# Optimization experiments

Measured on AMD Instinct MI355X. Metric: run time of the kernel, lower is better.

The kernel has to match this reference:

```python
import jax, jax.numpy as jnp
import numpy as np

N = 50000      # nodes
E = 800000     # edges
H = 4          # heads (all layers)
D = 64         # per-head out dim (n_hidden == n_classes == 64)
IN = 256       # in_feats; also H*D so identity residual is valid
NEG_SLOPE = 0.2


def setup_inputs() -> dict:
    key = jax.random.key(0)
    ks = jax.random.split(key, 16)
    x = jax.random.normal(ks[0], (N, IN), dtype=jnp.float32)
    src = jax.random.randint(ks[1], (E,), 0, N, dtype=jnp.int32)
    dst = jax.random.randint(ks[2], (E,), 0, N, dtype=jnp.int32)
    inp = {"x": x, "src": src, "dst": dst}
    fan_ins = [IN, H * D, H * D]  # layer input widths
    for i, fin in enumerate(fan_ins):
        s = 1.0 / np.sqrt(fin)
        inp[f"W{i}"] = jax.random.normal(ks[3 + 4 * i], (fin, H * D), dtype=jnp.float32) * s
        inp[f"al{i}"] = jax.random.normal(ks[4 + 4 * i], (H, D), dtype=jnp.float32) * s
        inp[f"ar{i}"] = jax.random.normal(ks[5 + 4 * i], (H, D), dtype=jnp.float32) * s
        inp[f"b{i}"] = jnp.zeros((H * D,), dtype=jnp.float32)
    return inp


def _gat_layer(h, src, dst, W, al, ar, b, residual, activate):
    # project: [N, in] @ [in, H*D] -> [N, H, D]
    feat = (h @ W).reshape(-1, H, D)
    el = jnp.sum(feat * al, axis=-1)            # [N, H]
    er = jnp.sum(feat * ar, axis=-1)            # [N, H]
    e = jax.nn.leaky_relu(el[src] + er[dst], NEG_SLOPE)  # [E, H]
    # edge softmax per destination node (stable: subtract per-dst max)
    emax = jax.ops.segment_max(e, dst, num_segments=N)  # [N, H]
    e = jnp.exp(e - emax[dst])
    denom = jax.ops.segment_sum(e, dst, num_segments=N)  # [N, H]
    alpha = e / denom[dst]                               # [E, H]
    # message + scatter-aggregate: [E, H, D] summed into [N, H, D]
    out = jax.ops.segment_sum(alpha[:, :, None] * feat[src], dst, num_segments=N)
    if residual:
        out = out + h.reshape(-1, H, D)  # identity residual (in == H*D)
    out = out + b.reshape(1, H, D)
    if activate:
        out = jax.nn.elu(out)
    return out


def reference(x, src, dst, W0, al0, ar0, b0, W1, al1, ar1, b1, W2, al2, ar2, b2):
    h = _gat_layer(x, src, dst, W0, al0, ar0, b0, False, True).reshape(N, H * D)
    h = _gat_layer(h, src, dst, W1, al1, ar1, b1, True, True).reshape(N, H * D)
    h = _gat_layer(h, src, dst, W2, al2, ar2, b2, True, False).mean(axis=1)  # [N, D]
    return h
```

## Files before the change

kernel.cpp:

```cpp
#include <hip/hip_runtime.h>
#include <math.h>

#define N_NODES 50000
#define N_EDGES 800000
#define HD 256
#define NHEAD 4
#define DH 64
#define NPAD 50048

typedef short bf16x8 __attribute__((ext_vector_type(8)));
typedef float f32x4 __attribute__((ext_vector_type(4)));

__device__ __forceinline__ unsigned short f2bf(float f) {
    unsigned u = __float_as_uint(f);
    return (unsigned short)((u + 0x7fffu + ((u >> 16) & 1u)) >> 16);
}
__device__ __forceinline__ float bf2f(unsigned short h) {
    return __uint_as_float((unsigned)h << 16);
}
__device__ __forceinline__ int origk(int k) {
    return (k & ~63) | ((k & 3) * 16 + ((k >> 2) & 15));
}

__global__ void packw_k(const float* __restrict__ W0, const float* __restrict__ W1,
                        const float* __restrict__ W2, unsigned short* __restrict__ Wp,
                        int* __restrict__ deg) {
    int blk = blockIdx.x;
    int L = blk >> 7, t = blk & 127;
    const float* W = L == 0 ? W0 : L == 1 ? W1 : W2;
    int nt = t >> 3, kt = t & 7;
    int lane = threadIdx.x;
    for (int i = blk * 64 + lane; i < 4 * NPAD; i += 384 * 64) deg[i] = 0;
    int col = nt * 16 + (lane & 15);
    int kb = kt * 32 + (lane >> 4) * 8;
    unsigned short v[8];
#pragma unroll
    for (int j = 0; j < 8; j++) {
        int k = kb + j;
        if (L > 0) k = origk(k);
        v[j] = f2bf(W[(size_t)k * 256 + col]);
    }
    *(bf16x8*)(Wp + ((size_t)(L * 128 + t) * 64 + lane) * 8) = *(bf16x8*)v;
}

__device__ __forceinline__ void mfma_tile(const unsigned short* Asl,
                                          const unsigned short* wbase,
                                          int lane, f32x4 acc[4][4]) {
#pragma unroll
    for (int kk = 0; kk < 8; kk++) {
        bf16x8 a[4], b[4];
#pragma unroll
        for (int m = 0; m < 4; m++) {
            int r = m * 16 + (lane & 15);
            int kb = kk * 32 + (lane >> 4) * 8;
            int byt = (r * 512 + kb * 2) ^ ((r & 7) << 4);
            a[m] = *(const bf16x8*)((const char*)Asl + byt);
        }
#pragma unroll
        for (int n = 0; n < 4; n++)
            b[n] = *(const bf16x8*)(wbase + ((size_t)(n * 8 + kk) * 64 + lane) * 8);
#pragma unroll
        for (int m = 0; m < 4; m++)
#pragma unroll
            for (int n = 0; n < 4; n++)
                acc[m][n] = __builtin_amdgcn_mfma_f32_16x16x32_bf16(a[m], b[n],
                                                                    acc[m][n], 0, 0, 0);
    }
}

__device__ __forceinline__ void epilogue_tile(f32x4 acc[4][4], int bm, int wv, int lane,
                                              const float* __restrict__ al,
                                              const float* __restrict__ ar,
                                              unsigned short* __restrict__ C,
                                              unsigned short* __restrict__ el,
                                              float* __restrict__ er, int M) {
    int rr = lane >> 4, cc = lane & 15;
    float alv[4], arv[4];
#pragma unroll
    for (int n = 0; n < 4; n++) {
        alv[n] = al[wv * 64 + n * 16 + cc];
        arv[n] = ar[wv * 64 + n * 16 + cc];
    }
    float vl[16], vr[16];
#pragma unroll
    for (int m = 0; m < 4; m++)
#pragma unroll
        for (int r = 0; r < 4; r++) {
            float ep = 0.f, rp = 0.f;
#pragma unroll
            for (int n = 0; n < 4; n++) {
                ep = fmaf(acc[m][n][r], alv[n], ep);
                rp = fmaf(acc[m][n][r], arv[n], rp);
            }
            vl[m * 4 + r] = ep;
            vr[m * 4 + r] = rp;
        }
    float l8[8], r8[8];
#pragma unroll
    for (int i = 0; i < 8; i++) {
        float xs = (cc & 1) ? vl[2 * i] : vl[2 * i + 1];
        float xk = (cc & 1) ? vl[2 * i + 1] : vl[2 * i];
        l8[i] = xk + __shfl_xor(xs, 1);
        float ys = (cc & 1) ? vr[2 * i] : vr[2 * i + 1];
        float yk = (cc & 1) ? vr[2 * i + 1] : vr[2 * i];
        r8[i] = yk + __shfl_xor(ys, 1);
    }
    float l4[4], r4[4];
#pragma unroll
    for (int i = 0; i < 4; i++) {
        float xs = (cc & 2) ? l8[2 * i] : l8[2 * i + 1];
        float xk = (cc & 2) ? l8[2 * i + 1] : l8[2 * i];
        l4[i] = xk + __shfl_xor(xs, 2);
        float ys = (cc & 2) ? r8[2 * i] : r8[2 * i + 1];
        float yk = (cc & 2) ? r8[2 * i + 1] : r8[2 * i];
        r4[i] = yk + __shfl_xor(ys, 2);
    }
    float l2[2], r2[2];
#pragma unroll
    for (int i = 0; i < 2; i++) {
        float xs = (cc & 4) ? l4[2 * i] : l4[2 * i + 1];
        float xk = (cc & 4) ? l4[2 * i + 1] : l4[2 * i];
        l2[i] = xk + __shfl_xor(xs, 4);
        float ys = (cc & 4) ? r4[2 * i] : r4[2 * i + 1];
        float yk = (cc & 4) ? r4[2 * i + 1] : r4[2 * i];
        r2[i] = yk + __shfl_xor(ys, 4);
    }
    {
        float xs = (cc & 8) ? l2[0] : l2[1];
        float xk = (cc & 8) ? l2[1] : l2[0];
        float lv = xk + __shfl_xor(xs, 8);
        float ys = (cc & 8) ? r2[0] : r2[1];
        float yk = (cc & 8) ? r2[1] : r2[0];
        float rv = yk + __shfl_xor(ys, 8);
        int row_e = bm + (cc >> 2) * 16 + rr * 4 + (cc & 3);
        if (row_e < M) {
            el[(size_t)row_e * NHEAD + wv] = f2bf(lv);
            er[(size_t)row_e * NHEAD + wv] = rv;
        }
    }
#pragma unroll
    for (int m = 0; m < 4; m++) {
#pragma unroll
        for (int r = 0; r < 4; r++) {
            int row = bm + m * 16 + rr * 4 + r;
            if (row < M) {
                unsigned short p4[4] = {f2bf(acc[m][0][r]), f2bf(acc[m][1][r]),
                                        f2bf(acc[m][2][r]), f2bf(acc[m][3][r])};
                *(ushort4*)(C + (size_t)row * 256 + wv * 64 + cc * 4) = *(ushort4*)p4;
            }
        }
    }
}

__global__ __launch_bounds__(256) void gemm0_k(const float* __restrict__ A,
                                               const unsigned short* __restrict__ Wp,
                                               const float* __restrict__ al,
                                               const float* __restrict__ ar,
                                               unsigned short* __restrict__ C,
                                               unsigned short* __restrict__ el,
                                               float* __restrict__ er, int M) {
    __shared__ unsigned short Asl[64 * 256];
    int tid = threadIdx.x, wv = tid >> 6, lane = tid & 63;
    int bm = blockIdx.x * 64;
#pragma unroll
    for (int i = 0; i < 8; i++) {
        int chunk = i * 256 + tid;
        int r = chunk >> 5, kc = (chunk & 31) * 8;
        float4 f0, f1;
        if (bm + r < M) {
            const float* p = A + (size_t)(bm + r) * 256 + kc;
            f0 = *(const float4*)p;
            f1 = *(const float4*)(p + 4);
        } else {
            f0 = f1 = make_float4(0.f, 0.f, 0.f, 0.f);
        }
        unsigned short tmp[8] = {f2bf(f0.x), f2bf(f0.y), f2bf(f0.z), f2bf(f0.w),
                                 f2bf(f1.x), f2bf(f1.y), f2bf(f1.z), f2bf(f1.w)};
        int b = (r * 512 + kc * 2) ^ ((r & 7) << 4);
        *(bf16x8*)((char*)Asl + b) = *(bf16x8*)tmp;
    }
    __syncthreads();
    const unsigned short* wbase = Wp + (size_t)(wv * 4) * 8 * 64 * 8;
    f32x4 acc[4][4] = {};
    mfma_tile(Asl, wbase, lane, acc);
    epilogue_tile(acc, bm, wv, lane, al, ar, C, el, er, M);
}

__global__ __launch_bounds__(256) void gemm2_k(const unsigned short* __restrict__ A,
                                               const unsigned short* __restrict__ Wp,
                                               const float* __restrict__ al,
                                               const float* __restrict__ ar,
                                               unsigned short* __restrict__ C,
                                               unsigned short* __restrict__ el,
                                               float* __restrict__ er, int M) {
    __shared__ unsigned short Asl[2][64 * 256];
    int tid = threadIdx.x, wv = tid >> 6, lane = tid & 63;
    int bm0 = blockIdx.x * 128, bm1 = bm0 + 64;
#pragma unroll
    for (int i = 0; i < 8; i++) {
        int chunk = i * 256 + tid;
        int r = chunk >> 5;
        int c16 = (chunk & 31) ^ (r & 7);
        int grow = bm0 + r; if (grow >= M) grow = M - 1;
        __builtin_amdgcn_global_load_lds(
            (const __attribute__((address_space(1))) unsigned int*)
                (A + (size_t)grow * 256 + c16 * 8),
            (__attribute__((address_space(3))) unsigned int*)
                ((char*)Asl[0] + (size_t)chunk * 16),
            16, 0, 0);
    }
#pragma unroll
    for (int i = 0; i < 8; i++) {
        int chunk = i * 256 + tid;
        int r = chunk >> 5;
        int c16 = (chunk & 31) ^ (r & 7);
        int grow = bm1 + r; if (grow >= M) grow = M - 1;
        __builtin_amdgcn_global_load_lds(
            (const __attribute__((address_space(1))) unsigned int*)
                (A + (size_t)grow * 256 + c16 * 8),
            (__attribute__((address_space(3))) unsigned int*)
                ((char*)Asl[1] + (size_t)chunk * 16),
            16, 0, 0);
    }
    asm volatile("s_waitcnt vmcnt(8)" ::: "memory");
    __builtin_amdgcn_sched_barrier(0);
    __builtin_amdgcn_s_barrier();
    const unsigned short* wbase = Wp + (size_t)(wv * 4) * 8 * 64 * 8;
    f32x4 acc[4][4] = {};
    mfma_tile(Asl[0], wbase, lane, acc);
    asm volatile("s_waitcnt vmcnt(0)" ::: "memory");
    __builtin_amdgcn_sched_barrier(0);
    __builtin_amdgcn_s_barrier();
    epilogue_tile(acc, bm0, wv, lane, al, ar, C, el, er, M);
    f32x4 acc2[4][4] = {};
    mfma_tile(Asl[1], wbase, lane, acc2);
    epilogue_tile(acc2, bm1, wv, lane, al, ar, C, el, er, M);
}

__global__ void hist_k(const int* __restrict__ dst, int* __restrict__ deg) {
    int t = blockIdx.x * 256 + threadIdx.x;
    int e = t * 2;
    int* mydeg = deg + (size_t)(threadIdx.x & 3) * NPAD;
    if (e + 1 < N_EDGES) {
        int2 d2 = *(const int2*)(dst + e);
        atomicAdd(&mydeg[d2.x], 1);
        atomicAdd(&mydeg[d2.y], 1);
    } else if (e < N_EDGES) {
        atomicAdd(&mydeg[dst[e]], 1);
    }
}

__global__ __launch_bounds__(1024) void scan1_k(const int* __restrict__ deg,
                                                int* __restrict__ rowptr,
                                                int* __restrict__ bsum) {
    __shared__ int wsum[16];
    int tid = threadIdx.x, lane = tid & 63, wv = tid >> 6;
    int i = blockIdx.x * 1024 + tid;
    int v = 0;
    if (i < N_NODES)
        v = deg[i] + deg[i + NPAD] + deg[i + 2 * NPAD] + deg[i + 3 * NPAD];
    int sc = v;
#pragma unroll
    for (int o = 1; o < 64; o <<= 1) {
        int t = __shfl_up(sc, o);
        if (lane >= o) sc += t;
    }
    if (lane == 63) wsum[wv] = sc;
    __syncthreads();
    if (wv == 0 && lane < 16) {
        int ws = wsum[lane];
#pragma unroll
        for (int o = 1; o < 16; o <<= 1) {
            int t = __shfl_up(ws, o);
            if (lane >= o) ws += t;
        }
        wsum[lane] = ws;
    }
    __syncthreads();
    int incl = sc + (wv > 0 ? wsum[wv - 1] : 0);
    if (i < N_NODES) rowptr[i + 1] = incl;
    if (tid == 1023) bsum[blockIdx.x] = incl;
}

__global__ __launch_bounds__(1024) void scan3_k(int* __restrict__ rowptr,
                                                const int* __restrict__ bsum,
                                                int* __restrict__ cursor, int nb) {
    __shared__ int boff_s;
    int tid = threadIdx.x;
    if (tid < 64) {
        int v = (tid < nb) ? bsum[tid] : 0;
        int sc = v;
#pragma unroll
        for (int o = 1; o < 64; o <<= 1) {
            int t = __shfl_up(sc, o);
            if ((tid & 63) >= o) sc += t;
        }
        if (tid == (int)blockIdx.x) boff_s = sc - v;
    }
    __syncthreads();
    int off = boff_s;
    int i = blockIdx.x * 1024 + tid;
    if (blockIdx.x == 0 && tid == 0) { rowptr[0] = 0; cursor[0] = 0; }
    if (i < N_NODES) {
        int v = rowptr[i + 1] + off;
        rowptr[i + 1] = v;
        if (i + 1 < N_NODES) cursor[i + 1] = v;
    }
}

__global__ void scatter_k(const int* __restrict__ src, const int* __restrict__ dst,
                          int* __restrict__ cursor, int* __restrict__ csr_src) {
    int e = (blockIdx.x * 256 + threadIdx.x) * 2;
    if (e + 1 < N_EDGES) {
        int2 s2 = *(const int2*)(src + e);
        int2 d2 = *(const int2*)(dst + e);
        csr_src[atomicAdd(&cursor[d2.x], 1)] = s2.x;
        csr_src[atomicAdd(&cursor[d2.y], 1)] = s2.y;
    } else if (e < N_EDGES) {
        csr_src[atomicAdd(&cursor[dst[e]], 1)] = src[e];
    }
}

template <int MODE>
__global__ __launch_bounds__(256) void agg_k(const int* __restrict__ rowptr,
                                             const int* __restrict__ csr_src,
                                             const unsigned short* __restrict__ el,
                                             const float* __restrict__ er,
                                             const unsigned short* __restrict__ feat,
                                             const unsigned short* __restrict__ resid,
                                             const float* __restrict__ bias,
                                             float* __restrict__ out,
                                             unsigned short* __restrict__ hb) {
    __shared__ int   ws_s[4][64];
    __shared__ float ws_w[4][4][68];
    int wv = threadIdx.x >> 6, lane = threadIdx.x & 63;
    int node = blockIdx.x * 4 + wv;
    if (node >= N_NODES) return;
    int beg = rowptr[node], end = rowptr[node + 1];
    float4 er4 = *(const float4*)(er + (size_t)node * 4);
    float4 acc0 = make_float4(0.f, 0.f, 0.f, 0.f);
    float4 acc1 = make_float4(0.f, 0.f, 0.f, 0.f);
    float4 den = make_float4(0.f, 0.f, 0.f, 0.f);
    int h = lane >> 4;
    int l8 = lane * 8;
    const char* fb = (const char*)feat;
    for (int base = beg; base < end; base += 64) {
        int j = base + lane;
        int soff = 0;
        float4 w = make_float4(0.f, 0.f, 0.f, 0.f);
        if (j < end) {
            int s = csr_src[j];
            soff = s << 9;
            ushort4 l4u = *(const ushort4*)(el + (size_t)s * 4);
            float vx = bf2f(l4u.x) + er4.x; vx = vx > 0.f ? vx : 0.2f * vx;
            float vy = bf2f(l4u.y) + er4.y; vy = vy > 0.f ? vy : 0.2f * vy;
            float vz = bf2f(l4u.z) + er4.z; vz = vz > 0.f ? vz : 0.2f * vz;
            float vw = bf2f(l4u.w) + er4.w; vw = vw > 0.f ? vw : 0.2f * vw;
            w.x = expf(vx); w.y = expf(vy); w.z = expf(vz); w.w = expf(vw);
            den.x += w.x; den.y += w.y; den.z += w.z; den.w += w.w;
        }
        ws_s[wv][lane] = soff;
        ws_w[wv][0][lane] = w.x;
        ws_w[wv][1][lane] = w.y;
        ws_w[wv][2][lane] = w.z;
        ws_w[wv][3][lane] = w.w;
        __builtin_amdgcn_wave_barrier();
        int cnt = end - base; if (cnt > 64) cnt = 64;
        int cnt4 = (cnt + 3) & ~3;
        for (int k = 0; k < cnt4; k += 4) {
            int4   so = *(const int4*)&ws_s[wv][k];
            float4 w4 = *(const float4*)&ws_w[wv][h][k];
            ushort4 u0 = *(const ushort4*)(fb + (so.x + l8));
            ushort4 u1 = *(const ushort4*)(fb + (so.y + l8));
            ushort4 u2 = *(const ushort4*)(fb + (so.z + l8));
            ushort4 u3 = *(const ushort4*)(fb + (so.w + l8));
            acc0.x = fmaf(w4.x, bf2f(u0.x), acc0.x);
            acc0.y = fmaf(w4.x, bf2f(u0.y), acc0.y);
            acc0.z = fmaf(w4.x, bf2f(u0.z), acc0.z);
            acc0.w = fmaf(w4.x, bf2f(u0.w), acc0.w);
            acc1.x = fmaf(w4.y, bf2f(u1.x), acc1.x);
            acc1.y = fmaf(w4.y, bf2f(u1.y), acc1.y);
            acc1.z = fmaf(w4.y, bf2f(u1.z), acc1.z);
            acc1.w = fmaf(w4.y, bf2f(u1.w), acc1.w);
            acc0.x = fmaf(w4.z, bf2f(u2.x), acc0.x);
            acc0.y = fmaf(w4.z, bf2f(u2.y), acc0.y);
            acc0.z = fmaf(w4.z, bf2f(u2.z), acc0.z);
            acc0.w = fmaf(w4.z, bf2f(u2.w), acc0.w);
            acc1.x = fmaf(w4.w, bf2f(u3.x), acc1.x);
            acc1.y = fmaf(w4.w, bf2f(u3.y), acc1.y);
            acc1.z = fmaf(w4.w, bf2f(u3.z), acc1.z);
            acc1.w = fmaf(w4.w, bf2f(u3.w), acc1.w);
        }
        __builtin_amdgcn_wave_barrier();
    }
    float4 acc;
    acc.x = acc0.x + acc1.x; acc.y = acc0.y + acc1.y;
    acc.z = acc0.z + acc1.z; acc.w = acc0.w + acc1.w;
#pragma unroll
    for (int o = 1; o < 64; o <<= 1) {
        den.x += __shfl_xor(den.x, o);
        den.y += __shfl_xor(den.y, o);
        den.z += __shfl_xor(den.z, o);
        den.w += __shfl_xor(den.w, o);
    }
    float den_me = h == 0 ? den.x : h == 1 ? den.y : h == 2 ? den.z : den.w;
    float r = den_me > 0.f ? 1.f / den_me : 0.f;
    int cc = lane & 15;
    float4 b4;
    b4.x = bias[h * 64 + 0 * 16 + cc];
    b4.y = bias[h * 64 + 1 * 16 + cc];
    b4.z = bias[h * 64 + 2 * 16 + cc];
    b4.w = bias[h * 64 + 3 * 16 + cc];
    float4 o4;
    o4.x = acc.x * r + b4.x;
    o4.y = acc.y * r + b4.y;
    o4.z = acc.z * r + b4.z;
    o4.w = acc.w * r + b4.w;
    if (MODE >= 1) {
        ushort4 r4 = *(const ushort4*)(resid + (size_t)node * HD + lane * 4);
        o4.x += bf2f(r4.x); o4.y += bf2f(r4.y);
        o4.z += bf2f(r4.z); o4.w += bf2f(r4.w);
    }
    if (MODE <= 1) {
        o4.x = o4.x > 0.f ? o4.x : expm1f(o4.x);
        o4.y = o4.y > 0.f ? o4.y : expm1f(o4.y);
        o4.z = o4.z > 0.f ? o4.z : expm1f(o4.z);
        o4.w = o4.w > 0.f ? o4.w : expm1f(o4.w);
        ushort4 hv;
        hv.x = f2bf(o4.x); hv.y = f2bf(o4.y); hv.z = f2bf(o4.z); hv.w = f2bf(o4.w);
        *(ushort4*)(hb + (size_t)node * HD + lane * 4) = hv;
    } else {
        o4.x += __shfl_xor(o4.x, 16); o4.x += __shfl_xor(o4.x, 32);
        o4.y += __shfl_xor(o4.y, 16); o4.y += __shfl_xor(o4.y, 32);
        o4.z += __shfl_xor(o4.z, 16); o4.z += __shfl_xor(o4.z, 32);
        o4.w += __shfl_xor(o4.w, 16); o4.w += __shfl_xor(o4.w, 32);
        if (lane < 16) {
            float* po = out + (size_t)node * DH;
            po[0 * 16 + lane] = o4.x * 0.25f;
            po[1 * 16 + lane] = o4.y * 0.25f;
            po[2 * 16 + lane] = o4.z * 0.25f;
            po[3 * 16 + lane] = o4.w * 0.25f;
        }
    }
}

extern "C" void kernel_launch(void* const* d_in, const int* in_sizes, int n_in,
                              void* d_out, int out_size, void* d_ws, size_t ws_size,
                              hipStream_t stream) {
    const float* x   = (const float*)d_in[0];
    const int*   src = (const int*)d_in[1];
    const int*   dst = (const int*)d_in[2];
    const float* W[3]  = {(const float*)d_in[3], (const float*)d_in[7],  (const float*)d_in[11]};
    const float* al[3] = {(const float*)d_in[4], (const float*)d_in[8],  (const float*)d_in[12]};
    const float* ar[3] = {(const float*)d_in[5], (const float*)d_in[9],  (const float*)d_in[13]};
    const float* bb[3] = {(const float*)d_in[6], (const float*)d_in[10], (const float*)d_in[14]};

    size_t big = (size_t)N_NODES * HD;
    unsigned short* featb = (unsigned short*)d_ws;
    unsigned short* hb1 = featb + big;
    unsigned short* hb2 = hb1 + big;
    unsigned short* el = hb2 + big;
    float* er = (float*)(el + (size_t)NPAD * NHEAD);
    int* deg     = (int*)(er + (size_t)NPAD * NHEAD);
    int* rowptr  = deg + 4 * NPAD;
    int* cursor  = rowptr + NPAD;
    int* csr_src = cursor + NPAD;
    int* bsum    = csr_src + N_EDGES;
    unsigned short* Wp = (unsigned short*)(bsum + 64);

    const int NB = (N_NODES + 1023) / 1024;

    packw_k<<<384, 64, 0, stream>>>(W[0], W[1], W[2], Wp, deg);
    hist_k<<<(N_EDGES / 2 + 255) / 256, 256, 0, stream>>>(dst, deg);
    scan1_k<<<NB, 1024, 0, stream>>>(deg, rowptr, bsum);
    scan3_k<<<NB, 1024, 0, stream>>>(rowptr, bsum, cursor, NB);
    scatter_k<<<(N_EDGES / 2 + 255) / 256, 256, 0, stream>>>(src, dst, cursor, csr_src);

    int g0grid = (N_NODES + 63) / 64;
    int g2grid = (N_NODES + 127) / 128;
    int agrid = (N_NODES + 3) / 4;

    gemm0_k<<<g0grid, 256, 0, stream>>>(x, Wp, al[0], ar[0], featb, el, er, N_NODES);
    agg_k<0><<<agrid, 256, 0, stream>>>(rowptr, csr_src, el, er, featb,
                                        nullptr, bb[0], nullptr, hb1);
    gemm2_k<<<g2grid, 256, 0, stream>>>(hb1, Wp + (size_t)1 * 128 * 64 * 8,
                                        al[1], ar[1], featb, el, er, N_NODES);
    agg_k<1><<<agrid, 256, 0, stream>>>(rowptr, csr_src, el, er, featb,
                                        hb1, bb[1], nullptr, hb2);
    gemm2_k<<<g2grid, 256, 0, stream>>>(hb2, Wp + (size_t)2 * 128 * 64 * 8,
                                        al[2], ar[2], featb, el, er, N_NODES);
    agg_k<2><<<agrid, 256, 0, stream>>>(rowptr, csr_src, el, er, featb,
                                        hb2, bb[2], (float*)d_out, nullptr);
}
```

Before: 327.1 us.

## Fuse weight packing with histogram and layer-0 GEMM with scan phase

Merges the weight-pack and degree-histogram kernels into one launch with block-range dispatch, and merges the layer-0 GEMM with the first scan pass. The deg zeroing moves to a memset, and the scan is now 1024 elements per 256-thread block, four per thread. The goal is fewer kernel launches and letting independent preprocessing work overlap on the GPU. The cost is a heterogeneous kernel whose shared-memory and register footprint is set by the GEMM branch, which may limit occupancy for the scan blocks.

```diff
diff --git a/kernel.cpp b/kernel.cpp
--- a/kernel.cpp
+++ b/kernel.cpp
@@ -8,6 +8,11 @@
 #define DH 64
 #define NPAD 50048
 
+#define GEMM_BLKS 782
+#define PACK_BLKS 96
+#define HIST_BLKS 1563
+#define NB 49
+
 typedef short bf16x8 __attribute__((ext_vector_type(8)));
 typedef float f32x4 __attribute__((ext_vector_type(4)));
 
@@ -20,27 +25,6 @@
 }
 __device__ __forceinline__ int origk(int k) {
     return (k & ~63) | ((k & 3) * 16 + ((k >> 2) & 15));
-}
-
-__global__ void packw_k(const float* __restrict__ W0, const float* __restrict__ W1,
-                        const float* __restrict__ W2, unsigned short* __restrict__ Wp,
-                        int* __restrict__ deg) {
-    int blk = blockIdx.x;
-    int L = blk >> 7, t = blk & 127;
-    const float* W = L == 0 ? W0 : L == 1 ? W1 : W2;
-    int nt = t >> 3, kt = t & 7;
-    int lane = threadIdx.x;
-    for (int i = blk * 64 + lane; i < 4 * NPAD; i += 384 * 64) deg[i] = 0;
-    int col = nt * 16 + (lane & 15);
-    int kb = kt * 32 + (lane >> 4) * 8;
-    unsigned short v[8];
-#pragma unroll
-    for (int j = 0; j < 8; j++) {
-        int k = kb + j;
-        if (L > 0) k = origk(k);
-        v[j] = f2bf(W[(size_t)k * 256 + col]);
-    }
-    *(bf16x8*)(Wp + ((size_t)(L * 128 + t) * 64 + lane) * 8) = *(bf16x8*)v;
 }
 
 __device__ __forceinline__ void mfma_tile(const unsigned short* Asl,
@@ -152,38 +136,151 @@
     }
 }
 
-__global__ __launch_bounds__(256) void gemm0_k(const float* __restrict__ A,
-                                               const unsigned short* __restrict__ Wp,
-                                               const float* __restrict__ al,
-                                               const float* __restrict__ ar,
-                                               unsigned short* __restrict__ C,
-                                               unsigned short* __restrict__ el,
-                                               float* __restrict__ er, int M) {
+__global__ __launch_bounds__(256) void fused_ph_k(const float* __restrict__ W0,
+                                                  const float* __restrict__ W1,
+                                                  const float* __restrict__ W2,
+                                                  unsigned short* __restrict__ Wp,
+                                                  const int* __restrict__ dst,
+                                                  int* __restrict__ deg) {
+    int blk = blockIdx.x, tid = threadIdx.x, wv = tid >> 6, lane = tid & 63;
+    if (blk < PACK_BLKS) {
+        int tile = blk * 4 + wv;
+        int L = tile >> 7, t = tile & 127;
+        const float* W = L == 0 ? W0 : L == 1 ? W1 : W2;
+        int nt = t >> 3, kt = t & 7;
+        int col = nt * 16 + (lane & 15);
+        int kb = kt * 32 + (lane >> 4) * 8;
+        unsigned short v[8];
+#pragma unroll
+        for (int j = 0; j < 8; j++) {
+            int k = kb + j;
+            if (L > 0) k = origk(k);
+            v[j] = f2bf(W[(size_t)k * 256 + col]);
+        }
+        *(bf16x8*)(Wp + ((size_t)(L * 128 + t) * 64 + lane) * 8) = *(bf16x8*)v;
+    } else {
+        int t = (blk - PACK_BLKS) * 256 + tid;
+        int e = t * 2;
+        int* mydeg = deg + (size_t)(tid & 3) * NPAD;
+        if (e + 1 < N_EDGES) {
+            int2 d2 = *(const int2*)(dst + e);
+            atomicAdd(&mydeg[d2.x], 1);
+            atomicAdd(&mydeg[d2.y], 1);
+        } else if (e < N_EDGES) {
+            atomicAdd(&mydeg[dst[e]], 1);
+        }
+    }
+}
+
+__global__ __launch_bounds__(256) void fused_gs_k(const float* __restrict__ A,
+                                                  const unsigned short* __restrict__ Wp,
+                                                  const float* __restrict__ al,
+                                                  const float* __restrict__ ar,
+                                                  unsigned short* __restrict__ C,
+                                                  unsigned short* __restrict__ el,
+                                                  float* __restrict__ er,
+                                                  const int* __restrict__ deg,
+                                                  int* __restrict__ rowptr,
+                                                  int* __restrict__ bsum, int M) {
     __shared__ unsigned short Asl[64 * 256];
-    int tid = threadIdx.x, wv = tid >> 6, lane = tid & 63;
-    int bm = blockIdx.x * 64;
-#pragma unroll
-    for (int i = 0; i < 8; i++) {
-        int chunk = i * 256 + tid;
-        int r = chunk >> 5, kc = (chunk & 31) * 8;
-        float4 f0, f1;
-        if (bm + r < M) {
-            const float* p = A + (size_t)(bm + r) * 256 + kc;
-            f0 = *(const float4*)p;
-            f1 = *(const float4*)(p + 4);
-        } else {
-            f0 = f1 = make_float4(0.f, 0.f, 0.f, 0.f);
-        }
-        unsigned short tmp[8] = {f2bf(f0.x), f2bf(f0.y), f2bf(f0.z), f2bf(f0.w),
-                                 f2bf(f1.x), f2bf(f1.y), f2bf(f1.z), f2bf(f1.w)};
-        int b = (r * 512 + kc * 2) ^ ((r & 7) << 4);
-        *(bf16x8*)((char*)Asl + b) = *(bf16x8*)tmp;
+    __shared__ int wsum2[4];
+    int blk = blockIdx.x, tid = threadIdx.x, wv = tid >> 6, lane = tid & 63;
+    if (blk < GEMM_BLKS) {
+        int bm = blk * 64;
+#pragma unroll
+        for (int i = 0; i < 8; i++) {
+            int chunk = i * 256 + tid;
+            int r = chunk >> 5, kc = (chunk & 31) * 8;
+            float4 f0, f1;
+            if (bm + r < M) {
+                const float* p = A + (size_t)(bm + r) * 256 + kc;
+                f0 = *(const float4*)p;
+                f1 = *(const float4*)(p + 4);
+            } else {
+                f0 = f1 = make_float4(0.f, 0.f, 0.f, 0.f);
+            }
+            unsigned short tmp[8] = {f2bf(f0.x), f2bf(f0.y), f2bf(f0.z), f2bf(f0.w),
+                                     f2bf(f1.x), f2bf(f1.y), f2bf(f1.z), f2bf(f1.w)};
+            int b = (r * 512 + kc * 2) ^ ((r & 7) << 4);
+            *(bf16x8*)((char*)Asl + b) = *(bf16x8*)tmp;
+        }
+        __syncthreads();
+        const unsigned short* wbase = Wp + (size_t)(wv * 4) * 8 * 64 * 8;
+        f32x4 acc[4][4] = {};
+        mfma_tile(Asl, wbase, lane, acc);
+        epilogue_tile(acc, bm, wv, lane, al, ar, C, el, er, M);
+    } else {
+        int sblk = blk - GEMM_BLKS;
+        int i0 = sblk * 1024 + tid * 4;
+        int v[4], p[4];
+#pragma unroll
+        for (int j = 0; j < 4; j++) {
+            int i = i0 + j;
+            v[j] = (i < N_NODES)
+                       ? deg[i] + deg[i + NPAD] + deg[i + 2 * NPAD] + deg[i + 3 * NPAD]
+                       : 0;
+        }
+        p[0] = v[0]; p[1] = p[0] + v[1]; p[2] = p[1] + v[2]; p[3] = p[2] + v[3];
+        int tot = p[3];
+        int sc = tot;
+#pragma unroll
+        for (int o = 1; o < 64; o <<= 1) {
+            int t = __shfl_up(sc, o);
+            if (lane >= o) sc += t;
+        }
+        if (lane == 63) wsum2[wv] = sc;
+        __syncthreads();
+        int woff = 0;
+#pragma unroll
+        for (int w = 0; w < 4; w++)
+            if (w < wv) woff += wsum2[w];
+        int excl = woff + sc - tot;
+#pragma unroll
+        for (int j = 0; j < 4; j++) {
+            int i = i0 + j;
+            if (i < N_NODES) rowptr[i + 1] = excl + p[j];
+        }
+        if (tid == 255) bsum[sblk] = excl + p[3];
+    }
+}
+
+__global__ __launch_bounds__(1024) void scan3_k(int* __restrict__ rowptr,
+                                                const int* __restrict__ bsum,
+                                                int* __restrict__ cursor, int nb) {
+    __shared__ int boff_s;
+    int tid = threadIdx.x;
+    if (tid < 64) {
+        int v = (tid < nb) ? bsum[tid] : 0;
+        int sc = v;
+#pragma unroll
+        for (int o = 1; o < 64; o <<= 1) {
+            int t = __shfl_up(sc, o);
+            if ((tid & 63) >= o) sc += t;
+        }
+        if (tid == (int)blockIdx.x) boff_s = sc - v;
     }
     __syncthreads();
-    const unsigned short* wbase = Wp + (size_t)(wv * 4) * 8 * 64 * 8;
-    f32x4 acc[4][4] = {};
-    mfma_tile(Asl, wbase, lane, acc);
-    epilogue_tile(acc, bm, wv, lane, al, ar, C, el, er, M);
+    int off = boff_s;
+    int i = blockIdx.x * 1024 + tid;
+    if (blockIdx.x == 0 && tid == 0) { rowptr[0] = 0; cursor[0] = 0; }
+    if (i < N_NODES) {
+        int v = rowptr[i + 1] + off;
+        rowptr[i + 1] = v;
+        if (i + 1 < N_NODES) cursor[i + 1] = v;
+    }
+}
+
+__global__ void scatter_k(const int* __restrict__ src, const int* __restrict__ dst,
+                          int* __restrict__ cursor, int* __restrict__ csr_src) {
+    int e = (blockIdx.x * 256 + threadIdx.x) * 2;
+    if (e + 1 < N_EDGES) {
+        int2 s2 = *(const int2*)(src + e);
+        int2 d2 = *(const int2*)(dst + e);
+        csr_src[atomicAdd(&cursor[d2.x], 1)] = s2.x;
+        csr_src[atomicAdd(&cursor[d2.y], 1)] = s2.y;
+    } else if (e < N_EDGES) {
+        csr_src[atomicAdd(&cursor[dst[e]], 1)] = src[e];
+    }
 }
 
 __global__ __launch_bounds__(256) void gemm2_k(const unsigned short* __restrict__ A,
@@ -235,90 +332,6 @@
     f32x4 acc2[4][4] = {};
     mfma_tile(Asl[1], wbase, lane, acc2);
     epilogue_tile(acc2, bm1, wv, lane, al, ar, C, el, er, M);
-}
-
-__global__ void hist_k(const int* __restrict__ dst, int* __restrict__ deg) {
-    int t = blockIdx.x * 256 + threadIdx.x;
-    int e = t * 2;
-    int* mydeg = deg + (size_t)(threadIdx.x & 3) * NPAD;
-    if (e + 1 < N_EDGES) {
-        int2 d2 = *(const int2*)(dst + e);
-        atomicAdd(&mydeg[d2.x], 1);
-        atomicAdd(&mydeg[d2.y], 1);
-    } else if (e < N_EDGES) {
-        atomicAdd(&mydeg[dst[e]], 1);
-    }
-}
-
-__global__ __launch_bounds__(1024) void scan1_k(const int* __restrict__ deg,
-                                                int* __restrict__ rowptr,
-                                                int* __restrict__ bsum) {
-    __shared__ int wsum[16];
-    int tid = threadIdx.x, lane = tid & 63, wv = tid >> 6;
-    int i = blockIdx.x * 1024 + tid;
-    int v = 0;
-    if (i < N_NODES)
-        v = deg[i] + deg[i + NPAD] + deg[i + 2 * NPAD] + deg[i + 3 * NPAD];
-    int sc = v;
-#pragma unroll
-    for (int o = 1; o < 64; o <<= 1) {
-        int t = __shfl_up(sc, o);
-        if (lane >= o) sc += t;
-    }
-    if (lane == 63) wsum[wv] = sc;
-    __syncthreads();
-    if (wv == 0 && lane < 16) {
-        int ws = wsum[lane];
-#pragma unroll
-        for (int o = 1; o < 16; o <<= 1) {
-            int t = __shfl_up(ws, o);
-            if (lane >= o) ws += t;
-        }
-        wsum[lane] = ws;
-    }
-    __syncthreads();
-    int incl = sc + (wv > 0 ? wsum[wv - 1] : 0);
-    if (i < N_NODES) rowptr[i + 1] = incl;
-    if (tid == 1023) bsum[blockIdx.x] = incl;
-}
-
-__global__ __launch_bounds__(1024) void scan3_k(int* __restrict__ rowptr,
-                                                const int* __restrict__ bsum,
-                                                int* __restrict__ cursor, int nb) {
-    __shared__ int boff_s;
-    int tid = threadIdx.x;
-    if (tid < 64) {
-        int v = (tid < nb) ? bsum[tid] : 0;
-        int sc = v;
-#pragma unroll
-        for (int o = 1; o < 64; o <<= 1) {
-            int t = __shfl_up(sc, o);
-            if ((tid & 63) >= o) sc += t;
-        }
-        if (tid == (int)blockIdx.x) boff_s = sc - v;
-    }
-    __syncthreads();
-    int off = boff_s;
-    int i = blockIdx.x * 1024 + tid;
-    if (blockIdx.x == 0 && tid == 0) { rowptr[0] = 0; cursor[0] = 0; }
-    if (i < N_NODES) {
-        int v = rowptr[i + 1] + off;
-        rowptr[i + 1] = v;
-        if (i + 1 < N_NODES) cursor[i + 1] = v;
-    }
-}
-
-__global__ void scatter_k(const int* __restrict__ src, const int* __restrict__ dst,
-                          int* __restrict__ cursor, int* __restrict__ csr_src) {
-    int e = (blockIdx.x * 256 + threadIdx.x) * 2;
-    if (e + 1 < N_EDGES) {
-        int2 s2 = *(const int2*)(src + e);
-        int2 d2 = *(const int2*)(dst + e);
-        csr_src[atomicAdd(&cursor[d2.x], 1)] = s2.x;
-        csr_src[atomicAdd(&cursor[d2.y], 1)] = s2.y;
-    } else if (e < N_EDGES) {
-        csr_src[atomicAdd(&cursor[dst[e]], 1)] = src[e];
-    }
 }
 
 template <int MODE>
@@ -468,19 +481,16 @@
     int* bsum    = csr_src + N_EDGES;
     unsigned short* Wp = (unsigned short*)(bsum + 64);
 
-    const int NB = (N_NODES + 1023) / 1024;
-
-    packw_k<<<384, 64, 0, stream>>>(W[0], W[1], W[2], Wp, deg);
-    hist_k<<<(N_EDGES / 2 + 255) / 256, 256, 0, stream>>>(dst, deg);
-    scan1_k<<<NB, 1024, 0, stream>>>(deg, rowptr, bsum);
+    hipMemsetAsync(deg, 0, (size_t)4 * NPAD * 4, stream);
+    fused_ph_k<<<PACK_BLKS + HIST_BLKS, 256, 0, stream>>>(W[0], W[1], W[2], Wp, dst, deg);
+    fused_gs_k<<<GEMM_BLKS + NB, 256, 0, stream>>>(x, Wp, al[0], ar[0], featb, el, er,
+                                                   deg, rowptr, bsum, N_NODES);
     scan3_k<<<NB, 1024, 0, stream>>>(rowptr, bsum, cursor, NB);
     scatter_k<<<(N_EDGES / 2 + 255) / 256, 256, 0, stream>>>(src, dst, cursor, csr_src);
 
-    int g0grid = (N_NODES + 63) / 64;
     int g2grid = (N_NODES + 127) / 128;
     int agrid = (N_NODES + 3) / 4;
 
-    gemm0_k<<<g0grid, 256, 0, stream>>>(x, Wp, al[0], ar[0], featb, el, er, N_NODES);
     agg_k<0><<<agrid, 256, 0, stream>>>(rowptr, csr_src, el, er, featb,
                                         nullptr, bb[0], nullptr, hb1);
     gemm2_k<<<g2grid, 256, 0, stream>>>(hb1, Wp + (size_t)1 * 128 * 64 * 8,
```

Measured after the change: 334.7 us. 2.3% more time.
